# Kernel optimization log

Measured on AMD Instinct MI355X. Metric: run time of the kernel, lower is better.

## Reference

```python
import jax, jax.numpy as jnp
import numpy as np

DIM = 1024
HEADS = 16
HEAD_DIM = DIM // HEADS
HIDDEN = int(DIM * 4.0)
EPS = 1e-5


def layernorm(x, w, b):
    m = jnp.mean(x, axis=-1, keepdims=True)
    v = jnp.var(x, axis=-1, keepdims=True)
    return (x - m) * jax.lax.rsqrt(v + EPS) * w + b


def apply_rope(t, pos):
    # t: [B, H, S, D], pos: [B, S] int
    half = t.shape[-1] // 2
    inv_freq = 1.0 / (10000.0 ** (jnp.arange(half, dtype=jnp.float32) / half))
    ang = pos.astype(jnp.float32)[:, None, :, None] * inv_freq  # [B,1,S,half]
    cos = jnp.cos(ang)
    sin = jnp.sin(ang)
    t1, t2 = t[..., :half], t[..., half:]
    return jnp.concatenate([t1 * cos - t2 * sin, t2 * cos + t1 * sin], axis=-1)


def setup_inputs() -> dict:
    key = jax.random.key(0)
    ks = jax.random.split(key, 10)
    B, S = 2, 2048
    x = jax.random.normal(ks[0], (B, S, DIM), dtype=jnp.float32)
    pos = jnp.sort(jax.random.randint(ks[1], (B, S), 0, 2048), axis=-1).astype(jnp.int32)
    def lin(k, fi, fo):
        return jax.random.normal(k, (fi, fo), dtype=jnp.float32) / np.sqrt(fi)
    return {
        "x": x,
        "pos": pos,
        "ln1_w": jnp.ones((DIM,), jnp.float32),
        "ln1_b": jnp.zeros((DIM,), jnp.float32),
        "qkv_w": lin(ks[2], DIM, 3 * DIM),
        "qkv_b": jnp.zeros((3 * DIM,), jnp.float32),
        "o_w": lin(ks[3], DIM, DIM),
        "o_b": jnp.zeros((DIM,), jnp.float32),
        "ln2_w": jnp.ones((DIM,), jnp.float32),
        "ln2_b": jnp.zeros((DIM,), jnp.float32),
        "mlp_w1": lin(ks[4], DIM, HIDDEN),
        "mlp_b1": jnp.zeros((HIDDEN,), jnp.float32),
        "mlp_w2": lin(ks[5], HIDDEN, DIM),
        "mlp_b2": jnp.zeros((DIM,), jnp.float32),
    }


def reference(x, pos, ln1_w, ln1_b, qkv_w, qkv_b, o_w, o_b, ln2_w, ln2_b, mlp_w1, mlp_b1, mlp_w2, mlp_b2):
    B, S, C = x.shape
    scale = HEAD_DIM ** -0.5
    xn = layernorm(x, ln1_w, ln1_b)
    qkv = (xn @ qkv_w + qkv_b).reshape(B, S, 3, HEADS, HEAD_DIM)
    qkv = jnp.transpose(qkv, (2, 0, 3, 1, 4))  # [3,B,H,S,D]
    q, k, v = qkv[0], qkv[1], qkv[2]
    q = apply_rope(q, pos)
    k = apply_rope(k, pos)
    scores = jnp.einsum("bhsd,bhtd->bhst", q, k) * scale
    probs = jax.nn.softmax(scores, axis=-1)
    attn = jnp.einsum("bhst,bhtd->bhsd", probs, v)
    attn = jnp.transpose(attn, (0, 2, 1, 3)).reshape(B, S, C)
    x = x + attn @ o_w + o_b
    xn2 = layernorm(x, ln2_w, ln2_b)
    h = jax.nn.gelu(xn2 @ mlp_w1 + mlp_b1, approximate=False)
    x = x + h @ mlp_w2 + mlp_b2
    return x
```

## Files before the change

### kernel.cpp

```cpp
#include <hip/hip_runtime.h>
#include <hip/hip_bf16.h>
#include <math.h>

#define DIMC 1024
#define HEADS 16
#define HD 64
#define HIDDEN 4096
#define BATCH 2
#define SEQ 2048
#define TOK (BATCH*SEQ)

typedef unsigned short u16;
typedef __attribute__((ext_vector_type(8))) short short8;
typedef __attribute__((ext_vector_type(4))) float f32x4;

__device__ __forceinline__ u16 f2bf(float f) {
  unsigned u = __float_as_uint(f);
  u += 0x7fff + ((u >> 16) & 1);
  return (u16)(u >> 16);
}
__device__ __forceinline__ float bf2f(u16 h) {
  return __uint_as_float(((unsigned)h) << 16);
}

__device__ __forceinline__ void gl_lds16(const void* g, void* l) {
  __builtin_amdgcn_global_load_lds(
      (__attribute__((address_space(1))) void*)g,
      (__attribute__((address_space(3))) void*)l, 16, 0, 0);
}

__device__ __forceinline__ const short8* lds_row128(const u16* base, int row, int chunk) {
  return (const short8*)((const char*)base + row * 128 + (((chunk) ^ (row & 7)) << 4));
}

__global__ __launch_bounds__(256) void ln_kernel(
    const float* __restrict__ x, const float* __restrict__ w,
    const float* __restrict__ b, u16* __restrict__ out)
{
  int row = blockIdx.x, tid = threadIdx.x;
  const float4* xr = (const float4*)(x + (size_t)row * DIMC);
  float4 v = xr[tid];
  float s = v.x + v.y + v.z + v.w;
  float s2 = v.x*v.x + v.y*v.y + v.z*v.z + v.w*v.w;
  for (int off = 32; off > 0; off >>= 1) {
    s  += __shfl_down(s, off);
    s2 += __shfl_down(s2, off);
  }
  __shared__ float red[8];
  int lane = tid & 63, wv = tid >> 6;
  if (lane == 0) { red[wv] = s; red[4 + wv] = s2; }
  __syncthreads();
  float S  = red[0] + red[1] + red[2] + red[3];
  float S2 = red[4] + red[5] + red[6] + red[7];
  float mean = S * (1.f / DIMC);
  float var  = S2 * (1.f / DIMC) - mean * mean;
  float inv  = rsqrtf(var + 1e-5f);
  int base = tid * 4;
  float vv[4] = {v.x, v.y, v.z, v.w};
#pragma unroll
  for (int j = 0; j < 4; ++j)
    out[(size_t)row * DIMC + base + j] = f2bf((vv[j] - mean) * inv * w[base + j] + b[base + j]);
}

__global__ __launch_bounds__(256) void transpose_cast(
    const float* __restrict__ W, u16* __restrict__ Wt, int K, int N)
{
  __shared__ float t[32][33];
  int n0 = blockIdx.x * 32, k0 = blockIdx.y * 32;
  for (int r = threadIdx.y; r < 32; r += 8)
    t[r][threadIdx.x] = W[(size_t)(k0 + r) * N + n0 + threadIdx.x];
  __syncthreads();
  for (int r = threadIdx.y; r < 32; r += 8)
    Wt[(size_t)(n0 + r) * K + k0 + threadIdx.x] = f2bf(t[threadIdx.x][r]);
}

template<int GELU>
__device__ __forceinline__ void gemm_lin_body(
    u16* shm, const u16* __restrict__ A, const u16* __restrict__ Bt,
    const float* __restrict__ bias, u16* __restrict__ outb, int M, int N, int K)
{
  int tid = threadIdx.x;
  int lane = tid & 63, w = tid >> 6;
  int wr = w >> 1, wc = w & 1;

  int nwg = gridDim.x * gridDim.y;
  int orig = blockIdx.y * gridDim.x + blockIdx.x;
  int wg = (orig & 7) * (nwg >> 3) + (orig >> 3);
  int gi = wg >> 4, wi = wg & 15;
  int gx4 = gridDim.x >> 2;
  int bx = (gi % gx4) * 4 + (wi & 3);
  int by = (gi / gx4) * 4 + (wi >> 2);
  int m0 = by * 128, n0 = bx * 128;

  f32x4 acc[4][4] = {};

  int offA[4], offB[4];
#pragma unroll
  for (int j = 0; j < 4; ++j) {
    int p = tid + j * 256, row = p >> 3, cl = (p & 7) ^ (row & 7);
    offA[j] = (m0 + row) * K + cl * 8;
    offB[j] = (n0 + row) * K + cl * 8;
  }
  int rofs = lane & 15, q4 = lane >> 4;
  int NT = K >> 6;
  u16* Bs = shm + 128 * 64;

  for (int t = 0; t < NT; ++t) {
#pragma unroll
    for (int j = 0; j < 4; ++j) {
      gl_lds16(A + offA[j] + t * 64, shm + (tid + j * 256) * 8);
      gl_lds16(Bt + offB[j] + t * 64, Bs + (tid + j * 256) * 8);
    }
    __syncthreads();
    {
      short8 af[4][2], bfr[4][2];
#pragma unroll
      for (int mm = 0; mm < 4; ++mm)
#pragma unroll
        for (int kk = 0; kk < 2; ++kk) {
          int row = wr * 64 + mm * 16 + rofs;
          af[mm][kk] = *(const short8*)((const char*)shm + row * 128 +
                                        ((((kk << 2) | q4) ^ (row & 7)) << 4));
        }
#pragma unroll
      for (int nn = 0; nn < 4; ++nn)
#pragma unroll
        for (int kk = 0; kk < 2; ++kk) {
          int row = wc * 64 + nn * 16 + rofs;
          bfr[nn][kk] = *(const short8*)((const char*)Bs + row * 128 +
                                         ((((kk << 2) | q4) ^ (row & 7)) << 4));
        }
#pragma unroll
      for (int kk = 0; kk < 2; ++kk)
#pragma unroll
        for (int mm = 0; mm < 4; ++mm)
#pragma unroll
          for (int nn = 0; nn < 4; ++nn)
            acc[mm][nn] = __builtin_amdgcn_mfma_f32_16x16x32_bf16(
                af[mm][kk], bfr[nn][kk], acc[mm][nn], 0, 0, 0);
    }
    __syncthreads();
  }

  u16* C = shm;
#pragma unroll
  for (int nn = 0; nn < 4; ++nn) {
    int ccol = wc * 64 + nn * 16 + rofs;
    float bv = bias[n0 + ccol];
#pragma unroll
    for (int mm = 0; mm < 4; ++mm)
#pragma unroll
      for (int r = 0; r < 4; ++r) {
        int crow = wr * 64 + mm * 16 + q4 * 4 + r;
        float v = acc[mm][nn][r] + bv;
        if (GELU) v = 0.5f * v * (1.f + erff(v * 0.70710678118f));
        C[crow * 128 + ccol] = f2bf(v);
      }
  }
  __syncthreads();
  for (int c = tid; c < 128 * 16; c += 256) {
    int row = c >> 4, off = (c & 15) * 8;
    *(short8*)(outb + (size_t)(m0 + row) * N + n0 + off) = *(const short8*)&C[row * 128 + off];
  }
}

__global__ __launch_bounds__(256) void gemm_qkv(
    const u16* __restrict__ A, const u16* __restrict__ Bt,
    const float* __restrict__ bias, u16* __restrict__ outb, int M, int N, int K)
{
  __shared__ u16 shm[128 * 64 * 2];
  gemm_lin_body<0>(shm, A, Bt, bias, outb, M, N, K);
}
__global__ __launch_bounds__(256) void gemm_mlp1(
    const u16* __restrict__ A, const u16* __restrict__ Bt,
    const float* __restrict__ bias, u16* __restrict__ outb, int M, int N, int K)
{
  __shared__ u16 shm[128 * 64 * 2];
  gemm_lin_body<1>(shm, A, Bt, bias, outb, M, N, K);
}

__device__ __forceinline__ void gemm_res_body(
    u16* shm, const u16* __restrict__ A, const u16* __restrict__ Bt,
    const float* __restrict__ bias, const float* __restrict__ res,
    float* __restrict__ outf, int M, int N, int K)
{
  constexpr int BM = 64, AMM = 2, HALF = 32, AJ = 2;
  constexpr int ASZ = BM * 64, BSZ = 128 * 64;
  int tid = threadIdx.x;
  int lane = tid & 63, w = tid >> 6;
  int wr = w >> 1, wc = w & 1;

  int nwg = gridDim.x * gridDim.y;
  int orig = blockIdx.y * gridDim.x + blockIdx.x;
  int wg = (orig & 7) * (nwg >> 3) + (orig >> 3);
  int gi = wg >> 4, wi = wg & 15;
  int gx4 = gridDim.x >> 2;
  int bx = (gi % gx4) * 4 + (wi & 3);
  int by = (gi / gx4) * 4 + (wi >> 2);
  int m0 = by * BM, n0 = bx * 128;

  f32x4 acc[AMM][4] = {};

  int offA[AJ], offB[4];
#pragma unroll
  for (int j = 0; j < AJ; ++j) {
    int p = tid + j * 256, row = p >> 3, cl = (p & 7) ^ (row & 7);
    offA[j] = (m0 + row) * K + cl * 8;
  }
#pragma unroll
  for (int j = 0; j < 4; ++j) {
    int p = tid + j * 256, row = p >> 3, cl = (p & 7) ^ (row & 7);
    offB[j] = (n0 + row) * K + cl * 8;
  }
  int rofs = lane & 15, q4 = lane >> 4;
  int NT = K >> 6;

  auto stage = [&](int buf, int t) {
    u16* Ab = shm + buf * ASZ;
    u16* Bb = shm + 2 * ASZ + buf * BSZ;
#pragma unroll
    for (int j = 0; j < AJ; ++j)
      gl_lds16(A + offA[j] + t * 64, Ab + (tid + j * 256) * 8);
#pragma unroll
    for (int j = 0; j < 4; ++j)
      gl_lds16(Bt + offB[j] + t * 64, Bb + (tid + j * 256) * 8);
  };
  auto compute = [&](int buf) {
    const char* Ab = (const char*)(shm + buf * ASZ);
    const char* Bb = (const char*)(shm + 2 * ASZ + buf * BSZ);
    short8 af[AMM][2], bfr[4][2];
#pragma unroll
    for (int mm = 0; mm < AMM; ++mm)
#pragma unroll
      for (int kk = 0; kk < 2; ++kk) {
        int row = wr * HALF + mm * 16 + rofs;
        af[mm][kk] = *(const short8*)(Ab + row * 128 +
                                      ((((kk << 2) | q4) ^ (row & 7)) << 4));
      }
#pragma unroll
    for (int nn = 0; nn < 4; ++nn)
#pragma unroll
      for (int kk = 0; kk < 2; ++kk) {
        int row = wc * 64 + nn * 16 + rofs;
        bfr[nn][kk] = *(const short8*)(Bb + row * 128 +
                                       ((((kk << 2) | q4) ^ (row & 7)) << 4));
      }
#pragma unroll
    for (int kk = 0; kk < 2; ++kk)
#pragma unroll
      for (int mm = 0; mm < AMM; ++mm)
#pragma unroll
        for (int nn = 0; nn < 4; ++nn)
          acc[mm][nn] = __builtin_amdgcn_mfma_f32_16x16x32_bf16(
              af[mm][kk], bfr[nn][kk], acc[mm][nn], 0, 0, 0);
  };

  stage(0, 0);
  __syncthreads();
  int cur = 0;
  for (int t = 0; t < NT; ++t) {
    if (t + 1 < NT) stage(cur ^ 1, t + 1);
    compute(cur);
    __syncthreads();
    cur ^= 1;
  }

  float* Cf = (float*)shm;
#pragma unroll
  for (int p = 0; p < 2; ++p) {
    if (wr == p) {
#pragma unroll
      for (int nn = 0; nn < 4; ++nn) {
        int ccol = wc * 64 + nn * 16 + rofs;
        float bv = bias[n0 + ccol];
#pragma unroll
        for (int mm = 0; mm < AMM; ++mm)
#pragma unroll
          for (int r = 0; r < 4; ++r)
            Cf[(mm * 16 + q4 * 4 + r) * 128 + ccol] = acc[mm][nn][r] + bv;
      }
    }
    __syncthreads();
    for (int c = tid; c < HALF * 32; c += 256) {
      int row = c >> 5, off = (c & 31) * 4;
      size_t idx = (size_t)(m0 + p * HALF + row) * N + n0 + off;
      float4 rv = *(const float4*)(res + idx);
      float4 cv = *(const float4*)&Cf[row * 128 + off];
      cv.x += rv.x; cv.y += rv.y; cv.z += rv.z; cv.w += rv.w;
      *(float4*)(outf + idx) = cv;
    }
    __syncthreads();
  }
}

__global__ __launch_bounds__(256) void gemm_oproj(
    const u16* __restrict__ A, const u16* __restrict__ Bt,
    const float* __restrict__ bias, const float* __restrict__ res,
    float* __restrict__ outf, int M, int N, int K)
{
  __shared__ u16 shm[(64 + 128) * 64 * 2];
  gemm_res_body(shm, A, Bt, bias, res, outf, M, N, K);
}
__global__ __launch_bounds__(256) void gemm_mlp2(
    const u16* __restrict__ A, const u16* __restrict__ Bt,
    const float* __restrict__ bias, const float* __restrict__ res,
    float* __restrict__ outf, int M, int N, int K)
{
  __shared__ u16 shm[(64 + 128) * 64 * 2];
  gemm_res_body(shm, A, Bt, bias, res, outf, M, N, K);
}

__global__ __launch_bounds__(256) void rope_split(
    const u16* __restrict__ qkv, const int* __restrict__ pos,
    u16* __restrict__ Q, u16* __restrict__ Kk, u16* __restrict__ Vt)
{
  int st = blockIdx.x, bh = blockIdx.y;
  int b = bh >> 4, hh = bh & 15;
  int s0 = st * 64;
  int tid = threadIdx.x;
  __shared__ u16 vtile[64][72];

  for (int i = tid; i < 64 * 32; i += 256) {
    int sl = i >> 5, dp = i & 31;
    int s = s0 + sl;
    float p = (float)pos[b * SEQ + s];
    float freq = exp2f((float)dp * -0.4152410118609203f);
    float ang = p * freq;
    float sn, c;
    __sincosf(ang, &sn, &c);
    const u16* qr = qkv + (size_t)(b * SEQ + s) * 3072 + hh * 64;
    float q1 = bf2f(qr[dp]),        q2 = bf2f(qr[dp + 32]);
    float k1 = bf2f(qr[1024 + dp]), k2 = bf2f(qr[1024 + dp + 32]);
    size_t ob = ((size_t)bh * SEQ + s) * HD;
    const float QS = 0.18033688011112042f;
    Q[ob + dp]       = f2bf((q1 * c - q2 * sn) * QS);
    Q[ob + dp + 32]  = f2bf((q2 * c + q1 * sn) * QS);
    Kk[ob + dp]      = f2bf(k1 * c - k2 * sn);
    Kk[ob + dp + 32] = f2bf(k2 * c + k1 * sn);
  }
  for (int i = tid; i < 64 * 64; i += 256) {
    int sl = i >> 6, d = i & 63;
    vtile[d][sl] = qkv[(size_t)(b * SEQ + s0 + sl) * 3072 + 2048 + hh * 64 + d];
  }
  __syncthreads();
  for (int i = tid; i < 64 * 64; i += 256) {
    int d = i >> 6, sl = i & 63;
    Vt[((size_t)bh * HD + d) * SEQ + s0 + sl] = vtile[d][sl];
  }
}

__global__ __launch_bounds__(256) void attn128(
    const u16* __restrict__ Q, const u16* __restrict__ K,
    const u16* __restrict__ Vt, u16* __restrict__ O)
{
  __shared__ u16 Ks[2][64 * 64];
  __shared__ u16 Vs[2][64 * 64];
  __shared__ u16 Ps[4 * 32 * 64];
  int qt = blockIdx.x, bh = blockIdx.y;
  int b = bh >> 4, hh = bh & 15;
  const u16* Qp = Q + ((size_t)bh * SEQ + qt * 128) * HD;
  const u16* Kp = K + (size_t)bh * SEQ * HD;
  const u16* Vp = Vt + (size_t)bh * HD * SEQ;
  int tid = threadIdx.x, lane = tid & 63, w = tid >> 6;
  int rofs = lane & 15, q4 = lane >> 4;
  int kofs = q4 * 8;

  short8 aq[2][2];
#pragma unroll
  for (int m = 0; m < 2; ++m)
#pragma unroll
    for (int h = 0; h < 2; ++h)
      aq[m][h] = *(const short8*)&Qp[(m * 64 + w * 16 + rofs) * HD + h * 32 + kofs];

  short8 ones;
#pragma unroll
  for (int j = 0; j < 8; ++j) ones[j] = (short)0x3F80;

  f32x4 o[2][4] = {};
  f32x4 lsum[2] = {};

  int srow = tid >> 3;
  int sg0 = ((tid & 7) ^ (srow & 7)) * 8;
  u16* pw = &Ps[w * 32 * 64];

#define A_STAGE(BUF, T0) do { \
    gl_lds16(Kp + (size_t)((T0) + srow) * HD + sg0, &Ks[BUF][tid * 8]); \
    gl_lds16(Kp + (size_t)((T0) + 32 + srow) * HD + sg0, &Ks[BUF][tid * 8 + 2048]); \
    gl_lds16(Vp + (size_t)srow * SEQ + (T0) + sg0, &Vs[BUF][tid * 8]); \
    gl_lds16(Vp + (size_t)(32 + srow) * SEQ + (T0) + sg0, &Vs[BUF][tid * 8 + 2048]); \
  } while (0)

  auto tile = [&](const u16* KsB, const u16* VsB) {
    f32x4 s[2][4] = {};
    short8 bk0[4], bk1[4];
#pragma unroll
    for (int n = 0; n < 4; ++n) {
      int krow = n * 16 + rofs;
      bk0[n] = *lds_row128(KsB, krow, q4);
      bk1[n] = *lds_row128(KsB, krow, 4 + q4);
    }
#pragma unroll
    for (int m = 0; m < 2; ++m)
#pragma unroll
      for (int n = 0; n < 4; ++n) {
        s[m][n] = __builtin_amdgcn_mfma_f32_16x16x32_bf16(aq[m][0], bk0[n], s[m][n], 0, 0, 0);
        s[m][n] = __builtin_amdgcn_mfma_f32_16x16x32_bf16(aq[m][1], bk1[n], s[m][n], 0, 0, 0);
      }
#pragma unroll
    for (int m = 0; m < 2; ++m)
#pragma unroll
      for (int n = 0; n < 4; ++n)
#pragma unroll
        for (int r = 0; r < 4; ++r) {
          int prow = m * 16 + q4 * 4 + r;
          int pbyte = (n * 16 + rofs) * 2;
          float p = __builtin_amdgcn_exp2f(s[m][n][r]);
          *(u16*)((char*)pw + prow * 128 + (pbyte ^ ((prow & 7) << 4))) = f2bf(p);
        }
    short8 pa[2][2];
#pragma unroll
    for (int m = 0; m < 2; ++m) {
      pa[m][0] = *lds_row128(pw, m * 16 + rofs, q4);
      pa[m][1] = *lds_row128(pw, m * 16 + rofs, 4 + q4);
    }
    short8 bv0[4], bv1[4];
#pragma unroll
    for (int n = 0; n < 4; ++n) {
      int vrow = n * 16 + rofs;
      bv0[n] = *lds_row128(VsB, vrow, q4);
      bv1[n] = *lds_row128(VsB, vrow, 4 + q4);
    }
#pragma unroll
    for (int m = 0; m < 2; ++m) {
      lsum[m] = __builtin_amdgcn_mfma_f32_16x16x32_bf16(pa[m][0], ones, lsum[m], 0, 0, 0);
      lsum[m] = __builtin_amdgcn_mfma_f32_16x16x32_bf16(pa[m][1], ones, lsum[m], 0, 0, 0);
#pragma unroll
      for (int n = 0; n < 4; ++n) {
        o[m][n] = __builtin_amdgcn_mfma_f32_16x16x32_bf16(pa[m][0], bv0[n], o[m][n], 0, 0, 0);
        o[m][n] = __builtin_amdgcn_mfma_f32_16x16x32_bf16(pa[m][1], bv1[n], o[m][n], 0, 0, 0);
      }
    }
  };

  A_STAGE(0, 0);
  __syncthreads();
  for (int t0 = 0; t0 < SEQ; t0 += 128) {
    if (t0 + 64 < SEQ) A_STAGE(1, t0 + 64);
    tile(Ks[0], Vs[0]);
    __syncthreads();
    if (t0 + 128 < SEQ) A_STAGE(0, t0 + 128);
    tile(Ks[1], Vs[1]);
    __syncthreads();
  }
#undef A_STAGE

#pragma unroll
  for (int m = 0; m < 2; ++m)
#pragma unroll
    for (int r = 0; r < 4; ++r) {
      float inv = 1.f / lsum[m][r];
      int rr = m * 64 + w * 16 + q4 * 4 + r;
#pragma unroll
      for (int n = 0; n < 4; ++n)
        Ps[rr * 64 + n * 16 + rofs] = f2bf(o[m][n][r] * inv);
    }
  __syncthreads();
  for (int c = tid; c < 128 * 8; c += 256) {
    int row = c >> 3, off = (c & 7) * 8;
    int sq = qt * 128 + row;
    *(short8*)(O + ((size_t)b * SEQ + sq) * DIMC + hh * 64 + off) = *(const short8*)&Ps[row * 64 + off];
  }
}

extern "C" void kernel_launch(void* const* d_in, const int* in_sizes, int n_in,
                              void* d_out, int out_size, void* d_ws, size_t ws_size,
                              hipStream_t stream) {
  const float* x     = (const float*)d_in[0];
  const int*   pos   = (const int*)  d_in[1];
  const float* ln1_w = (const float*)d_in[2];
  const float* ln1_b = (const float*)d_in[3];
  const float* qkv_w = (const float*)d_in[4];
  const float* qkv_b = (const float*)d_in[5];
  const float* o_w   = (const float*)d_in[6];
  const float* o_b   = (const float*)d_in[7];
  const float* ln2_w = (const float*)d_in[8];
  const float* ln2_b = (const float*)d_in[9];
  const float* w1    = (const float*)d_in[10];
  const float* b1    = (const float*)d_in[11];
  const float* w2    = (const float*)d_in[12];
  const float* b2    = (const float*)d_in[13];
  float* out = (float*)d_out;

  char* ws = (char*)d_ws;
  u16* WqkvT = (u16*)(ws + 0);
  u16* WoT   = (u16*)(ws + 6291456);
  u16* W1T   = (u16*)(ws + 8388608);
  u16* W2T   = (u16*)(ws + 16777216);
  u16* xn    = (u16*)(ws + 25165824);
  u16* qkvbf = (u16*)(ws + 33554432);
  u16* Qb    = (u16*)(ws + 58720256);
  u16* Kb    = (u16*)(ws + 67108864);
  u16* Vtb   = (u16*)(ws + 75497472);
  u16* attnb = (u16*)(ws + 83886080);
  u16* hbuf  = (u16*)(ws + 25165824);
  float* x2  = (float*)(ws + 58720256);
  u16* xn2   = (u16*)(ws + 75497472);

  transpose_cast<<<dim3(3072/32, 1024/32), dim3(32, 8), 0, stream>>>(qkv_w, WqkvT, 1024, 3072);
  transpose_cast<<<dim3(1024/32, 1024/32), dim3(32, 8), 0, stream>>>(o_w,  WoT,  1024, 1024);
  transpose_cast<<<dim3(4096/32, 1024/32), dim3(32, 8), 0, stream>>>(w1,   W1T,  1024, 4096);
  transpose_cast<<<dim3(1024/32, 4096/32), dim3(32, 8), 0, stream>>>(w2,   W2T,  4096, 1024);

  ln_kernel<<<TOK, 256, 0, stream>>>(x, ln1_w, ln1_b, xn);
  gemm_qkv<<<dim3(24, 32), 256, 0, stream>>>(xn, WqkvT, qkv_b, qkvbf, 4096, 3072, 1024);
  rope_split<<<dim3(32, 32), 256, 0, stream>>>(qkvbf, pos, Qb, Kb, Vtb);
  attn128<<<dim3(16, 32), 256, 0, stream>>>(Qb, Kb, Vtb, attnb);
  gemm_oproj<<<dim3(8, 64), 256, 0, stream>>>(attnb, WoT, o_b, x, x2, 4096, 1024, 1024);
  ln_kernel<<<TOK, 256, 0, stream>>>(x2, ln2_w, ln2_b, xn2);
  gemm_mlp1<<<dim3(32, 32), 256, 0, stream>>>(xn2, W1T, b1, hbuf, 4096, 4096, 1024);
  gemm_mlp2<<<dim3(8, 64), 256, 0, stream>>>(hbuf, W2T, b2, x2, out, 4096, 1024, 4096);
}
```

Baseline: 257.2 us.

## Double-buffer QKV/MLP1 GEMMs with 64-row tiles and remap attention block order

The QKV and MLP1 GEMMs move from a single-buffered 128x128 tile to a 64x128 tile with double-buffered shared memory. The next K-slice is loaded while the current one is computed, and the grid is doubled to keep the same coverage. The smaller tile gives twice as many workgroups for the ~256 CUs, but each tile reuses loaded data less. The attention kernel's block index is also remapped so that blocks running together span different batch-heads, which changes cache and XCD locality.

Measured after the change: 254.2 us. About the same (-1.2%).

```diff
diff --git a/kernel.cpp b/kernel.cpp
--- a/kernel.cpp
+++ b/kernel.cpp
@@ -75,10 +75,12 @@
 }
 
 template<int GELU>
-__device__ __forceinline__ void gemm_lin_body(
+__device__ __forceinline__ void gemm64_body(
     u16* shm, const u16* __restrict__ A, const u16* __restrict__ Bt,
     const float* __restrict__ bias, u16* __restrict__ outb, int M, int N, int K)
 {
+  constexpr int BM = 64, AMM = 2, HALF = 32, AJ = 2;
+  constexpr int ASZ = BM * 64, BSZ = 128 * 64;
   int tid = threadIdx.x;
   int lane = tid & 63, w = tid >> 6;
   int wr = w >> 1, wc = w & 1;
@@ -90,56 +92,72 @@
   int gx4 = gridDim.x >> 2;
   int bx = (gi % gx4) * 4 + (wi & 3);
   int by = (gi / gx4) * 4 + (wi >> 2);
-  int m0 = by * 128, n0 = bx * 128;
-
-  f32x4 acc[4][4] = {};
-
-  int offA[4], offB[4];
+  int m0 = by * BM, n0 = bx * 128;
+
+  f32x4 acc[AMM][4] = {};
+
+  int offA[AJ], offB[4];
+#pragma unroll
+  for (int j = 0; j < AJ; ++j) {
+    int p = tid + j * 256, row = p >> 3, cl = (p & 7) ^ (row & 7);
+    offA[j] = (m0 + row) * K + cl * 8;
+  }
 #pragma unroll
   for (int j = 0; j < 4; ++j) {
     int p = tid + j * 256, row = p >> 3, cl = (p & 7) ^ (row & 7);
-    offA[j] = (m0 + row) * K + cl * 8;
     offB[j] = (n0 + row) * K + cl * 8;
   }
   int rofs = lane & 15, q4 = lane >> 4;
   int NT = K >> 6;
-  u16* Bs = shm + 128 * 64;
-
+
+  auto stage = [&](int buf, int t) {
+    u16* Ab = shm + buf * ASZ;
+    u16* Bb = shm + 2 * ASZ + buf * BSZ;
+#pragma unroll
+    for (int j = 0; j < AJ; ++j)
+      gl_lds16(A + offA[j] + t * 64, Ab + (tid + j * 256) * 8);
+#pragma unroll
+    for (int j = 0; j < 4; ++j)
+      gl_lds16(Bt + offB[j] + t * 64, Bb + (tid + j * 256) * 8);
+  };
+  auto compute = [&](int buf) {
+    const char* Ab = (const char*)(shm + buf * ASZ);
+    const char* Bb = (const char*)(shm + 2 * ASZ + buf * BSZ);
+    short8 af[AMM][2], bfr[4][2];
+#pragma unroll
+    for (int mm = 0; mm < AMM; ++mm)
+#pragma unroll
+      for (int kk = 0; kk < 2; ++kk) {
+        int row = wr * HALF + mm * 16 + rofs;
+        af[mm][kk] = *(const short8*)(Ab + row * 128 +
+                                      ((((kk << 2) | q4) ^ (row & 7)) << 4));
+      }
+#pragma unroll
+    for (int nn = 0; nn < 4; ++nn)
+#pragma unroll
+      for (int kk = 0; kk < 2; ++kk) {
+        int row = wc * 64 + nn * 16 + rofs;
+        bfr[nn][kk] = *(const short8*)(Bb + row * 128 +
+                                       ((((kk << 2) | q4) ^ (row & 7)) << 4));
+      }
+#pragma unroll
+    for (int kk = 0; kk < 2; ++kk)
+#pragma unroll
+      for (int mm = 0; mm < AMM; ++mm)
+#pragma unroll
+        for (int nn = 0; nn < 4; ++nn)
+          acc[mm][nn] = __builtin_amdgcn_mfma_f32_16x16x32_bf16(
+              af[mm][kk], bfr[nn][kk], acc[mm][nn], 0, 0, 0);
+  };
+
+  stage(0, 0);
+  __syncthreads();
+  int cur = 0;
   for (int t = 0; t < NT; ++t) {
-#pragma unroll
-    for (int j = 0; j < 4; ++j) {
-      gl_lds16(A + offA[j] + t * 64, shm + (tid + j * 256) * 8);
-      gl_lds16(Bt + offB[j] + t * 64, Bs + (tid + j * 256) * 8);
-    }
+    if (t + 1 < NT) stage(cur ^ 1, t + 1);
+    compute(cur);
     __syncthreads();
-    {
-      short8 af[4][2], bfr[4][2];
-#pragma unroll
-      for (int mm = 0; mm < 4; ++mm)
-#pragma unroll
-        for (int kk = 0; kk < 2; ++kk) {
-          int row = wr * 64 + mm * 16 + rofs;
-          af[mm][kk] = *(const short8*)((const char*)shm + row * 128 +
-                                        ((((kk << 2) | q4) ^ (row & 7)) << 4));
-        }
-#pragma unroll
-      for (int nn = 0; nn < 4; ++nn)
-#pragma unroll
-        for (int kk = 0; kk < 2; ++kk) {
-          int row = wc * 64 + nn * 16 + rofs;
-          bfr[nn][kk] = *(const short8*)((const char*)Bs + row * 128 +
-                                         ((((kk << 2) | q4) ^ (row & 7)) << 4));
-        }
-#pragma unroll
-      for (int kk = 0; kk < 2; ++kk)
-#pragma unroll
-        for (int mm = 0; mm < 4; ++mm)
-#pragma unroll
-          for (int nn = 0; nn < 4; ++nn)
-            acc[mm][nn] = __builtin_amdgcn_mfma_f32_16x16x32_bf16(
-                af[mm][kk], bfr[nn][kk], acc[mm][nn], 0, 0, 0);
-    }
-    __syncthreads();
+    cur ^= 1;
   }
 
   u16* C = shm;
@@ -148,17 +166,17 @@
     int ccol = wc * 64 + nn * 16 + rofs;
     float bv = bias[n0 + ccol];
 #pragma unroll
-    for (int mm = 0; mm < 4; ++mm)
+    for (int mm = 0; mm < AMM; ++mm)
 #pragma unroll
       for (int r = 0; r < 4; ++r) {
-        int crow = wr * 64 + mm * 16 + q4 * 4 + r;
+        int crow = wr * HALF + mm * 16 + q4 * 4 + r;
         float v = acc[mm][nn][r] + bv;
         if (GELU) v = 0.5f * v * (1.f + erff(v * 0.70710678118f));
         C[crow * 128 + ccol] = f2bf(v);
       }
   }
   __syncthreads();
-  for (int c = tid; c < 128 * 16; c += 256) {
+  for (int c = tid; c < BM * 16; c += 256) {
     int row = c >> 4, off = (c & 15) * 8;
     *(short8*)(outb + (size_t)(m0 + row) * N + n0 + off) = *(const short8*)&C[row * 128 + off];
   }
@@ -168,15 +186,15 @@
     const u16* __restrict__ A, const u16* __restrict__ Bt,
     const float* __restrict__ bias, u16* __restrict__ outb, int M, int N, int K)
 {
-  __shared__ u16 shm[128 * 64 * 2];
-  gemm_lin_body<0>(shm, A, Bt, bias, outb, M, N, K);
+  __shared__ u16 shm[(64 + 128) * 64 * 2];
+  gemm64_body<0>(shm, A, Bt, bias, outb, M, N, K);
 }
 __global__ __launch_bounds__(256) void gemm_mlp1(
     const u16* __restrict__ A, const u16* __restrict__ Bt,
     const float* __restrict__ bias, u16* __restrict__ outb, int M, int N, int K)
 {
-  __shared__ u16 shm[128 * 64 * 2];
-  gemm_lin_body<1>(shm, A, Bt, bias, outb, M, N, K);
+  __shared__ u16 shm[(64 + 128) * 64 * 2];
+  gemm64_body<1>(shm, A, Bt, bias, outb, M, N, K);
 }
 
 __device__ __forceinline__ void gemm_res_body(
@@ -356,7 +374,9 @@
   __shared__ u16 Ks[2][64 * 64];
   __shared__ u16 Vs[2][64 * 64];
   __shared__ u16 Ps[4 * 32 * 64];
-  int qt = blockIdx.x, bh = blockIdx.y;
+  int orig = blockIdx.y * gridDim.x + blockIdx.x;
+  int bh = (orig & 7) * 4 + ((orig >> 3) & 3);
+  int qt = orig >> 5;
   int b = bh >> 4, hh = bh & 15;
   const u16* Qp = Q + ((size_t)bh * SEQ + qt * 128) * HD;
   const u16* Kp = K + (size_t)bh * SEQ * HD;
@@ -512,11 +532,11 @@
   transpose_cast<<<dim3(1024/32, 4096/32), dim3(32, 8), 0, stream>>>(w2,   W2T,  4096, 1024);
 
   ln_kernel<<<TOK, 256, 0, stream>>>(x, ln1_w, ln1_b, xn);
-  gemm_qkv<<<dim3(24, 32), 256, 0, stream>>>(xn, WqkvT, qkv_b, qkvbf, 4096, 3072, 1024);
+  gemm_qkv<<<dim3(24, 64), 256, 0, stream>>>(xn, WqkvT, qkv_b, qkvbf, 4096, 3072, 1024);
   rope_split<<<dim3(32, 32), 256, 0, stream>>>(qkvbf, pos, Qb, Kb, Vtb);
   attn128<<<dim3(16, 32), 256, 0, stream>>>(Qb, Kb, Vtb, attnb);
   gemm_oproj<<<dim3(8, 64), 256, 0, stream>>>(attnb, WoT, o_b, x, x2, 4096, 1024, 1024);
   ln_kernel<<<TOK, 256, 0, stream>>>(x2, ln2_w, ln2_b, xn2);
-  gemm_mlp1<<<dim3(32, 32), 256, 0, stream>>>(xn2, W1T, b1, hbuf, 4096, 4096, 1024);
+  gemm_mlp1<<<dim3(32, 64), 256, 0, stream>>>(xn2, W1T, b1, hbuf, 4096, 4096, 1024);
   gemm_mlp2<<<dim3(8, 64), 256, 0, stream>>>(hbuf, W2T, b2, x2, out, 4096, 1024, 4096);
 }
```
